# Kernel optimization log

Measured on AMD Instinct MI355X. Metric: run time of the kernel, lower is better.

## Reference

```python
import jax, jax.numpy as jnp
import numpy as np

N_HEADS = 12

def setup_inputs() -> dict:
    key = jax.random.key(0)
    ks = jax.random.split(key, 3)
    B, C, T = 4, 768, 2048
    x = jax.random.normal(ks[0], (B, C, T), dtype=jnp.float32)
    mask = jnp.ones((B, 1, 1, T), dtype=jnp.int32)  # all valid; masked_fill where mask==0
    Wqkv = jax.random.normal(ks[1], (3 * C, C), dtype=jnp.float32) * 0.02
    bqkv = jnp.zeros((3 * C,), dtype=jnp.float32)
    Wout = jax.random.normal(ks[2], (C, C), dtype=jnp.float32) * 0.02
    bout = jnp.zeros((C,), dtype=jnp.float32)
    return {"x": x, "mask": mask, "Wqkv": Wqkv, "bqkv": bqkv, "Wout": Wout, "bout": bout}


def reference(x, mask, Wqkv, bqkv, Wout, bout):
    B, C, T = x.shape
    H = N_HEADS
    d = C // H
    scale = 1.0 / jnp.sqrt(jnp.asarray(d, x.dtype))
    # 1x1 Conv1d == per-timestep matmul over channels
    qkv = jnp.einsum('oc,bct->bot', Wqkv, x) + bqkv[None, :, None]  # [B,3C,T]
    # channel dim splits as [3, H, d] per the torch view(B,3,H,d,T)
    qkv = qkv.reshape(B, 3, H, d, T).transpose(0, 1, 2, 4, 3)       # [B,3,H,T,d]
    q, k, v = qkv[:, 0], qkv[:, 1], qkv[:, 2]
    score = jnp.einsum('bhtd,bhsd->bhts', q, k) * scale             # [B,H,T,T]
    score = jnp.where(mask == 0, jnp.asarray(-10000.0, score.dtype), score)
    attn = jax.nn.softmax(score, axis=-1)  # dropout: eval mode (identity)
    o = jnp.einsum('bhts,bhsd->bhtd', attn, v)                      # [B,H,T,d]
    o = o.transpose(0, 1, 3, 2).reshape(B, C, T)                    # [B,C,T]
    return jnp.einsum('oc,bct->bot', Wout, o) + bout[None, :, None]
```

## Files before the change

### kernel.cpp

```cpp
#include <hip/hip_runtime.h>
#include <hip/hip_bf16.h>
#include <stdint.h>

#define B_   4
#define C_   768
#define T_   2048
#define H_   12
#define D_   64
#define O3_  2304

typedef __attribute__((ext_vector_type(4))) float f32x4;
typedef __attribute__((ext_vector_type(8))) short bf16x8;

__device__ __forceinline__ unsigned short f2bf(float f) {
  union { float f; unsigned int u; } v; v.f = f;
  unsigned int r = v.u + 0x7fffu + ((v.u >> 16) & 1u);
  return (unsigned short)(r >> 16);
}

__device__ __forceinline__ unsigned int pack2bf(float a, float b) {
  __hip_bfloat162 h2 = __float22bfloat162_rn(make_float2(a, b));
  union { __hip_bfloat162 h; unsigned int u; } cv; cv.h = h2;
  return cv.u;
}

__device__ __forceinline__ float fexp2(float x) {
#if __has_builtin(__builtin_amdgcn_exp2f)
  return __builtin_amdgcn_exp2f(x);
#else
  return exp2f(x);
#endif
}

__device__ __forceinline__ void async16(const void* g, void* lds) {
#if __has_builtin(__builtin_amdgcn_global_load_lds)
  __builtin_amdgcn_global_load_lds((const __attribute__((address_space(1))) void*)g,
                                   (__attribute__((address_space(3))) void*)lds, 16, 0, 0);
#else
  int lane = threadIdx.x & 63;
  *((uint4*)((char*)lds + lane * 16)) = *((const uint4*)g);
#endif
}


__global__ void cvt_f32_bf16(const float* __restrict__ in,
                             unsigned short* __restrict__ out, int n4) {
  int i = blockIdx.x * 256 + threadIdx.x;
  if (i < n4) {
    float4 f = ((const float4*)in)[i];
    ushort4 o;
    o.x = f2bf(f.x); o.y = f2bf(f.y); o.z = f2bf(f.z); o.w = f2bf(f.w);
    ((ushort4*)out)[i] = o;
  }
}

__global__ void make_bias(const int* __restrict__ mask, float* __restrict__ mbias, int n) {
  int i = blockIdx.x * 256 + threadIdx.x;
  if (i < n) mbias[i] = (mask[i] == 0) ? -14426.950408f : 0.0f;
}

__global__ void transpose_x(const float* __restrict__ x,
                            unsigned short* __restrict__ xT) {
  __shared__ unsigned short tile[32][33];
  int b = blockIdx.z;
  int c0 = blockIdx.y * 32;
  int t0 = blockIdx.x * 32;
  int tid = threadIdx.x;
  {
    int cl = tid >> 3;
    int tl = (tid & 7) * 4;
    float4 f = *(const float4*)(x + ((size_t)b * C_ + c0 + cl) * T_ + t0 + tl);
    tile[tl + 0][cl] = f2bf(f.x);
    tile[tl + 1][cl] = f2bf(f.y);
    tile[tl + 2][cl] = f2bf(f.z);
    tile[tl + 3][cl] = f2bf(f.w);
  }
  __syncthreads();
  {
    int tl = tid >> 3;
    int cl = (tid & 7) * 4;
    ushort4 o;
    o.x = tile[tl][cl + 0]; o.y = tile[tl][cl + 1];
    o.z = tile[tl][cl + 2]; o.w = tile[tl][cl + 3];
    *(ushort4*)(xT + ((size_t)b * T_ + t0 + tl) * C_ + c0 + cl) = o;
  }
}

__global__ __launch_bounds__(256)
void gemm_qkv(const unsigned short* __restrict__ xT,
              const unsigned short* __restrict__ W1,
              const float* __restrict__ bqkv,
              unsigned short* __restrict__ Qb,
              unsigned short* __restrict__ Kb,
              unsigned short* __restrict__ Vb) {
  __shared__ unsigned short sA[2][128 * 32];
  __shared__ unsigned short sB[2][128 * 32];

  const int b   = blockIdx.z;
  const int o0  = blockIdx.y * 128;
  const int t0  = blockIdx.x * 128;
  const int tid = threadIdx.x;
  const int wave = tid >> 6, lane = tid & 63;
  const int q = lane >> 4, ln = lane & 15;
  const int tw = wave >> 1, ow = wave & 1;

  const unsigned short* Ax = xT + (size_t)b * T_ * C_;
  const int srow = lane >> 2;
  const int scol = (lane & 3) * 8;

  const f32x4 ZERO = {0.f, 0.f, 0.f, 0.f};
  f32x4 acc[4][4];
#pragma unroll
  for (int mi = 0; mi < 4; ++mi)
#pragma unroll
    for (int ni = 0; ni < 4; ++ni) acc[mi][ni] = ZERO;

#pragma unroll
  for (int j = 0; j < 2; ++j) {
    const int chunk = wave * 2 + j;
    const int row = chunk * 16 + srow;
    async16(Ax + (size_t)(t0 + row) * C_ + scol, &sA[0][chunk * 512]);
    async16(W1 + (size_t)(o0 + row) * C_ + scol, &sB[0][chunk * 512]);
  }

  for (int i = 0; i < 24; ++i) {
    const int buf = i & 1;
    __syncthreads();
    if (i < 23) {
      const int k0 = (i + 1) * 32;
#pragma unroll
      for (int j = 0; j < 2; ++j) {
        const int chunk = wave * 2 + j;
        const int row = chunk * 16 + srow;
        async16(Ax + (size_t)(t0 + row) * C_ + k0 + scol, &sA[buf ^ 1][chunk * 512]);
        async16(W1 + (size_t)(o0 + row) * C_ + k0 + scol, &sB[buf ^ 1][chunk * 512]);
      }
    }

    bf16x8 aF[4], bF[4];
#pragma unroll
    for (int mi = 0; mi < 4; ++mi)
      aF[mi] = *(const bf16x8*)(&sA[buf][(tw * 64 + mi * 16 + ln) * 32 + q * 8]);
#pragma unroll
    for (int ni = 0; ni < 4; ++ni)
      bF[ni] = *(const bf16x8*)(&sB[buf][(ow * 64 + ni * 16 + ln) * 32 + q * 8]);
#pragma unroll
    for (int mi = 0; mi < 4; ++mi)
#pragma unroll
      for (int ni = 0; ni < 4; ++ni)
        acc[mi][ni] = __builtin_amdgcn_mfma_f32_16x16x32_bf16(aF[mi], bF[ni], acc[mi][ni], 0, 0, 0);
  }

  const float QSCL = 0.125f * 1.44269504f;
#pragma unroll
  for (int ni = 0; ni < 4; ++ni) {
    const int o = o0 + ow * 64 + ni * 16 + ln;
    const float bias = bqkv[o];
    const int which = o / C_;
    const int rem = o - which * C_;
    const int bh = b * H_ + (rem >> 6);
    const int dd = rem & 63;
#pragma unroll
    for (int mi = 0; mi < 4; ++mi) {
      const int tb = t0 + tw * 64 + mi * 16 + q * 4;
      f32x4 v = acc[mi][ni];
      if (which == 0) {
#pragma unroll
        for (int r = 0; r < 4; ++r)
          Qb[((size_t)bh * T_ + tb + r) * D_ + dd] = f2bf((v[r] + bias) * QSCL);
      } else if (which == 1) {
#pragma unroll
        for (int r = 0; r < 4; ++r) {
          const int s = tb + r;
          const int cp = (dd >> 3) ^ (s & 7);
          Kb[((size_t)bh * T_ + s) * 64 + (cp << 3) + (dd & 7)] = f2bf(v[r] + bias);
        }
      } else {
        const int tile = tb >> 6, si = tb & 63;
        const int cp = (si >> 3) ^ (dd & 7);
        ushort4 pk;
        pk.x = f2bf(v[0] + bias);
        pk.y = f2bf(v[1] + bias);
        pk.z = f2bf(v[2] + bias);
        pk.w = f2bf(v[3] + bias);
        *(ushort4*)(Vb + (((size_t)bh * 32 + tile) * 64 + dd) * 64 + (cp << 3) + (si & 7)) = pk;
      }
    }
  }
}

__global__ __launch_bounds__(256, 3)
void attn(const unsigned short* __restrict__ Qb,
          const unsigned short* __restrict__ Kb,
          const unsigned short* __restrict__ Vb,
          const float* __restrict__ mbias,
          unsigned short* __restrict__ Ob) {
  __shared__ __align__(16) char smem[53248];
  unsigned short* sK0 = (unsigned short*)smem;
  unsigned short* sV0 = (unsigned short*)(smem + 16384);

  const int id = blockIdx.x;
  const int bh = id % 48;
  const int tblk = id / 48;
  const int b = bh / H_, h = bh % H_;
  const int tid = threadIdx.x, wave = tid >> 6, lane = tid & 63;
  const int q = lane >> 4, ln = lane & 15;
  const int wj = wave & 1, si = wave >> 1;
  const int t0w = tblk * 128 + wj * 64;
  unsigned short* sPw = (unsigned short*)(smem + 32768 + wave * 5120);

  bf16x8 Qa[4][2];
#pragma unroll
  for (int tt = 0; tt < 4; ++tt) {
    const unsigned short* qrow = Qb + ((size_t)bh * T_ + t0w + tt * 16 + ln) * D_;
    Qa[tt][0] = *(const bf16x8*)(qrow + q * 8);
    Qa[tt][1] = *(const bf16x8*)(qrow + 32 + q * 8);
  }

  const f32x4 ZERO = {0.f, 0.f, 0.f, 0.f};
  f32x4 Oacc[4][4];
  f32x4 lacc[4];
#pragma unroll
  for (int dt = 0; dt < 4; ++dt)
#pragma unroll
    for (int tt = 0; tt < 4; ++tt) Oacc[dt][tt] = ZERO;
#pragma unroll
  for (int tt = 0; tt < 4; ++tt) lacc[tt] = ZERO;

  const short one_s = (ln == 0) ? (short)0x3F80 : (short)0;
  bf16x8 ones;
#pragma unroll
  for (int j = 0; j < 8; ++j) ones[j] = one_s;

  const unsigned short* gK = Kb + (size_t)bh * T_ * 64;
  const unsigned short* gV = Vb + (size_t)bh * 32 * 4096;

#pragma unroll
  for (int j = 0; j < 2; ++j) {
    const int chunk = wave * 2 + j;
    async16(gK + chunk * 512 + lane * 8, sK0 + chunk * 512);
    async16(gV + chunk * 512 + lane * 8, sV0 + chunk * 512);
  }

  for (int it = 0; it < 32; ++it) {
    const int buf = it & 1;
    __syncthreads();
    if (it < 31) {
      const unsigned short* k = gK + (it + 1) * 4096;
      const unsigned short* v = gV + (it + 1) * 4096;
      unsigned short* dK = sK0 + (buf ^ 1) * 4096;
      unsigned short* dV = sV0 + (buf ^ 1) * 4096;
#pragma unroll
      for (int j = 0; j < 2; ++j) {
        const int chunk = wave * 2 + j;
        async16(k + chunk * 512 + lane * 8, dK + chunk * 512);
        async16(v + chunk * 512 + lane * 8, dV + chunk * 512);
      }
    }

    const int s0 = it * 64;
    const float bvl = mbias[b * T_ + s0 + lane];
    const bool anymask = (__ballot(bvl != 0.0f) != 0ull);
    const unsigned short* sKc = sK0 + buf * 4096;
    const unsigned short* sVc = sV0 + buf * 4096;

#pragma unroll
    for (int sb = 0; sb < 2; ++sb) {
      const unsigned short* krow = sKc + (si * 32 + sb * 16 + ln) * 64;
      bf16x8 kf0 = *(const bf16x8*)(krow + ((q ^ (ln & 7)) << 3));
      bf16x8 kf1 = *(const bf16x8*)(krow + (((4 + q) ^ (ln & 7)) << 3));
      f32x4 bb = ZERO;
      if (anymask) bb = *(const f32x4*)(mbias + b * T_ + s0 + si * 32 + sb * 16 + q * 4);
#pragma unroll
      for (int tt = 0; tt < 4; ++tt) {
        f32x4 p0 = __builtin_amdgcn_mfma_f32_16x16x32_bf16(kf0, Qa[tt][0], ZERO, 0, 0, 0);
        f32x4 sc = __builtin_amdgcn_mfma_f32_16x16x32_bf16(kf1, Qa[tt][1], p0, 0, 0, 0);
        if (anymask) {
#pragma unroll
          for (int r = 0; r < 4; ++r) sc[r] += bb[r];
        }
        uint2 w;
        w.x = pack2bf(fexp2(sc[0]), fexp2(sc[1]));
        w.y = pack2bf(fexp2(sc[2]), fexp2(sc[3]));
        *(uint2*)(sPw + (tt * 16 + ln) * 40 + sb * 16 + q * 4) = w;
      }
    }

    bf16x8 vf[4];
#pragma unroll
    for (int dt = 0; dt < 4; ++dt)
      vf[dt] = *(const bf16x8*)(sVc + (dt * 16 + ln) * 64 +
                                (((si * 4 + q) ^ (ln & 7)) << 3));
#pragma unroll
    for (int tt = 0; tt < 4; ++tt) {
      bf16x8 pf = *(const bf16x8*)(sPw + (tt * 16 + ln) * 40 + q * 8);
      lacc[tt] = __builtin_amdgcn_mfma_f32_16x16x32_bf16(ones, pf, lacc[tt], 0, 0, 0);
#pragma unroll
      for (int dt = 0; dt < 4; ++dt)
        Oacc[dt][tt] = __builtin_amdgcn_mfma_f32_16x16x32_bf16(vf[dt], pf, Oacc[dt][tt], 0, 0, 0);
    }
  }

  __syncthreads();
  float* fbuf = (float*)smem;
  float* lbuf = (float*)(smem + 34816);
  if (si == 1) {
#pragma unroll
    for (int tt = 0; tt < 4; ++tt) {
#pragma unroll
      for (int dt = 0; dt < 4; ++dt)
        *(f32x4*)(fbuf + ((size_t)(wj * 64 + tt * 16 + ln)) * 68 + dt * 16 + q * 4) = Oacc[dt][tt];
      if (q == 0) lbuf[wj * 64 + tt * 16 + ln] = lacc[tt][0];
    }
  }
  __syncthreads();
  if (si == 0) {
#pragma unroll
    for (int tt = 0; tt < 4; ++tt) {
      const float lv = __shfl(lacc[tt][0], ln, 64) + lbuf[wj * 64 + tt * 16 + ln];
      const float inv = 1.0f / lv;
      const int t = t0w + tt * 16 + ln;
#pragma unroll
      for (int dt = 0; dt < 4; ++dt) {
        f32x4 o = Oacc[dt][tt];
        f32x4 p = *(const f32x4*)(fbuf + ((size_t)(wj * 64 + tt * 16 + ln)) * 68 + dt * 16 + q * 4);
        ushort4 pk;
        pk.x = f2bf((o[0] + p[0]) * inv);
        pk.y = f2bf((o[1] + p[1]) * inv);
        pk.z = f2bf((o[2] + p[2]) * inv);
        pk.w = f2bf((o[3] + p[3]) * inv);
        *(ushort4*)(Ob + ((size_t)b * T_ + t) * C_ + h * D_ + dt * 16 + q * 4) = pk;
      }
    }
  }
}

__global__ __launch_bounds__(256)
void gemm_out(const unsigned short* __restrict__ Ob,
              const unsigned short* __restrict__ W2,
              const float* __restrict__ bout,
              float* __restrict__ out) {
  __shared__ unsigned short sA[2][128 * 32];
  __shared__ unsigned short sB[2][128 * 32];

  const int b   = blockIdx.z;
  const int o0  = blockIdx.y * 128;
  const int t0  = blockIdx.x * 128;
  const int tid = threadIdx.x;
  const int wave = tid >> 6, lane = tid & 63;
  const int q = lane >> 4, ln = lane & 15;
  const int tw = wave >> 1, ow = wave & 1;

  const unsigned short* Bo = Ob + (size_t)b * T_ * C_;
  const int srow = lane >> 2;
  const int scol = (lane & 3) * 8;

  const f32x4 ZERO = {0.f, 0.f, 0.f, 0.f};
  f32x4 acc[4][4];
#pragma unroll
  for (int mi = 0; mi < 4; ++mi)
#pragma unroll
    for (int ni = 0; ni < 4; ++ni) acc[mi][ni] = ZERO;

#pragma unroll
  for (int j = 0; j < 2; ++j) {
    const int chunk = wave * 2 + j;
    const int row = chunk * 16 + srow;
    async16(W2 + (size_t)(o0 + row) * C_ + scol, &sA[0][chunk * 512]);
    async16(Bo + (size_t)(t0 + row) * C_ + scol, &sB[0][chunk * 512]);
  }

  for (int i = 0; i < 24; ++i) {
    const int buf = i & 1;
    __syncthreads();
    if (i < 23) {
      const int k0 = (i + 1) * 32;
#pragma unroll
      for (int j = 0; j < 2; ++j) {
        const int chunk = wave * 2 + j;
        const int row = chunk * 16 + srow;
        async16(W2 + (size_t)(o0 + row) * C_ + k0 + scol, &sA[buf ^ 1][chunk * 512]);
        async16(Bo + (size_t)(t0 + row) * C_ + k0 + scol, &sB[buf ^ 1][chunk * 512]);
      }
    }

    bf16x8 aF[4], bF[4];
#pragma unroll
    for (int mi = 0; mi < 4; ++mi)
      aF[mi] = *(const bf16x8*)(&sA[buf][(tw * 64 + mi * 16 + ln) * 32 + q * 8]);
#pragma unroll
    for (int ni = 0; ni < 4; ++ni)
      bF[ni] = *(const bf16x8*)(&sB[buf][(ow * 64 + ni * 16 + ln) * 32 + q * 8]);
#pragma unroll
    for (int mi = 0; mi < 4; ++mi)
#pragma unroll
      for (int ni = 0; ni < 4; ++ni)
        acc[mi][ni] = __builtin_amdgcn_mfma_f32_16x16x32_bf16(aF[mi], bF[ni], acc[mi][ni], 0, 0, 0);
  }

#pragma unroll
  for (int mi = 0; mi < 4; ++mi) {
    const int ob = o0 + tw * 64 + mi * 16 + q * 4;
#pragma unroll
    for (int ni = 0; ni < 4; ++ni) {
      const int t = t0 + ow * 64 + ni * 16 + ln;
      f32x4 v = acc[mi][ni];
#pragma unroll
      for (int r = 0; r < 4; ++r)
        out[((size_t)b * C_ + ob + r) * T_ + t] = v[r] + bout[ob + r];
    }
  }
}


extern "C" void kernel_launch(void* const* d_in, const int* in_sizes, int n_in,
                              void* d_out, int out_size, void* d_ws, size_t ws_size,
                              hipStream_t stream) {
  (void)in_sizes; (void)n_in; (void)out_size; (void)ws_size;
  const float* x    = (const float*)d_in[0];
  const int*   mask = (const int*)d_in[1];
  const float* Wqkv = (const float*)d_in[2];
  const float* bqkv = (const float*)d_in[3];
  const float* Wout = (const float*)d_in[4];
  const float* bout = (const float*)d_in[5];
  float* out = (float*)d_out;

  const size_t szHead = (size_t)B_ * H_ * T_ * D_;
  const size_t szBTC  = (size_t)B_ * T_ * C_;
  unsigned short* Qb  = (unsigned short*)d_ws;
  unsigned short* Kb  = Qb + szHead;
  unsigned short* Vb  = Kb + szHead;
  unsigned short* Ob  = Vb + szHead;
  unsigned short* xT  = Ob + szBTC;
  unsigned short* W1b = xT + szBTC;
  unsigned short* W2b = W1b + (size_t)O3_ * C_;
  float* mbias        = (float*)(W2b + (size_t)C_ * C_);

  cvt_f32_bf16<<<dim3((O3_ * C_ / 4 + 255) / 256), 256, 0, stream>>>(Wqkv, W1b, O3_ * C_ / 4);
  cvt_f32_bf16<<<dim3((C_ * C_ / 4 + 255) / 256), 256, 0, stream>>>(Wout, W2b, C_ * C_ / 4);
  make_bias<<<dim3((B_ * T_ + 255) / 256), 256, 0, stream>>>(mask, mbias, B_ * T_);
  transpose_x<<<dim3(T_ / 32, C_ / 32, B_), 256, 0, stream>>>(x, xT);
  gemm_qkv<<<dim3(T_ / 128, O3_ / 128, B_), 256, 0, stream>>>(xT, W1b, bqkv, Qb, Kb, Vb);
  attn<<<dim3(768), 256, 0, stream>>>(Qb, Kb, Vb, mbias, Ob);
  gemm_out<<<dim3(T_ / 128, C_ / 128, B_), 256, 0, stream>>>(Ob, W2b, bout, out);
}
```

Baseline: 236.3 us.

## Keep softmax probabilities in registers via permlane swaps instead of LDS round-trip

```diff
diff --git a/kernel.cpp b/kernel.cpp
--- a/kernel.cpp
+++ b/kernel.cpp
@@ -195,7 +195,7 @@
           const unsigned short* __restrict__ Vb,
           const float* __restrict__ mbias,
           unsigned short* __restrict__ Ob) {
-  __shared__ __align__(16) char smem[53248];
+  __shared__ __align__(16) char smem[32768];
   unsigned short* sK0 = (unsigned short*)smem;
   unsigned short* sV0 = (unsigned short*)(smem + 16384);
 
@@ -205,27 +205,25 @@
   const int b = bh / H_, h = bh % H_;
   const int tid = threadIdx.x, wave = tid >> 6, lane = tid & 63;
   const int q = lane >> 4, ln = lane & 15;
-  const int wj = wave & 1, si = wave >> 1;
-  const int t0w = tblk * 128 + wj * 64;
-  unsigned short* sPw = (unsigned short*)(smem + 32768 + wave * 5120);
-
-  bf16x8 Qa[4][2];
-#pragma unroll
-  for (int tt = 0; tt < 4; ++tt) {
+  const int t0w = tblk * 128 + wave * 32;
+
+  bf16x8 Qa[2][2];
+#pragma unroll
+  for (int tt = 0; tt < 2; ++tt) {
     const unsigned short* qrow = Qb + ((size_t)bh * T_ + t0w + tt * 16 + ln) * D_;
     Qa[tt][0] = *(const bf16x8*)(qrow + q * 8);
     Qa[tt][1] = *(const bf16x8*)(qrow + 32 + q * 8);
   }
 
   const f32x4 ZERO = {0.f, 0.f, 0.f, 0.f};
-  f32x4 Oacc[4][4];
-  f32x4 lacc[4];
+  f32x4 Oacc[4][2];
+  f32x4 lacc[2];
 #pragma unroll
   for (int dt = 0; dt < 4; ++dt)
 #pragma unroll
-    for (int tt = 0; tt < 4; ++tt) Oacc[dt][tt] = ZERO;
-#pragma unroll
-  for (int tt = 0; tt < 4; ++tt) lacc[tt] = ZERO;
+    for (int tt = 0; tt < 2; ++tt) Oacc[dt][tt] = ZERO;
+#pragma unroll
+  for (int tt = 0; tt < 2; ++tt) lacc[tt] = ZERO;
 
   const short one_s = (ln == 0) ? (short)0x3F80 : (short)0;
   bf16x8 ones;
@@ -264,73 +262,78 @@
     const unsigned short* sKc = sK0 + buf * 4096;
     const unsigned short* sVc = sV0 + buf * 4096;
 
-#pragma unroll
-    for (int sb = 0; sb < 2; ++sb) {
-      const unsigned short* krow = sKc + (si * 32 + sb * 16 + ln) * 64;
-      bf16x8 kf0 = *(const bf16x8*)(krow + ((q ^ (ln & 7)) << 3));
-      bf16x8 kf1 = *(const bf16x8*)(krow + (((4 + q) ^ (ln & 7)) << 3));
-      f32x4 bb = ZERO;
-      if (anymask) bb = *(const f32x4*)(mbias + b * T_ + s0 + si * 32 + sb * 16 + q * 4);
-#pragma unroll
-      for (int tt = 0; tt < 4; ++tt) {
-        f32x4 p0 = __builtin_amdgcn_mfma_f32_16x16x32_bf16(kf0, Qa[tt][0], ZERO, 0, 0, 0);
-        f32x4 sc = __builtin_amdgcn_mfma_f32_16x16x32_bf16(kf1, Qa[tt][1], p0, 0, 0, 0);
-        if (anymask) {
-#pragma unroll
-          for (int r = 0; r < 4; ++r) sc[r] += bb[r];
+    bf16x8 pf[2][2];
+#pragma unroll
+    for (int kc = 0; kc < 2; ++kc) {
+      bf16x8 kf[2][2];
+#pragma unroll
+      for (int sb = 0; sb < 2; ++sb) {
+        const unsigned short* krow = sKc + (kc * 32 + sb * 16 + ln) * 64;
+        kf[sb][0] = *(const bf16x8*)(krow + ((q ^ (ln & 7)) << 3));
+        kf[sb][1] = *(const bf16x8*)(krow + (((4 + q) ^ (ln & 7)) << 3));
+      }
+#pragma unroll
+      for (int tt = 0; tt < 2; ++tt) {
+        f32x4 sc[2];
+#pragma unroll
+        for (int sb = 0; sb < 2; ++sb) {
+          f32x4 p0 = __builtin_amdgcn_mfma_f32_16x16x32_bf16(kf[sb][0], Qa[tt][0], ZERO, 0, 0, 0);
+          sc[sb]   = __builtin_amdgcn_mfma_f32_16x16x32_bf16(kf[sb][1], Qa[tt][1], p0, 0, 0, 0);
+          if (anymask) {
+            f32x4 bb = *(const f32x4*)(mbias + b * T_ + s0 + kc * 32 + sb * 16 + q * 4);
+#pragma unroll
+            for (int r = 0; r < 4; ++r) sc[sb][r] += bb[r];
+          }
         }
-        uint2 w;
-        w.x = pack2bf(fexp2(sc[0]), fexp2(sc[1]));
-        w.y = pack2bf(fexp2(sc[2]), fexp2(sc[3]));
-        *(uint2*)(sPw + (tt * 16 + ln) * 40 + sb * 16 + q * 4) = w;
-      }
-    }
-
-    bf16x8 vf[4];
-#pragma unroll
-    for (int dt = 0; dt < 4; ++dt)
-      vf[dt] = *(const bf16x8*)(sVc + (dt * 16 + ln) * 64 +
-                                (((si * 4 + q) ^ (ln & 7)) << 3));
-#pragma unroll
-    for (int tt = 0; tt < 4; ++tt) {
-      bf16x8 pf = *(const bf16x8*)(sPw + (tt * 16 + ln) * 40 + q * 8);
-      lacc[tt] = __builtin_amdgcn_mfma_f32_16x16x32_bf16(ones, pf, lacc[tt], 0, 0, 0);
-#pragma unroll
-      for (int dt = 0; dt < 4; ++dt)
-        Oacc[dt][tt] = __builtin_amdgcn_mfma_f32_16x16x32_bf16(vf[dt], pf, Oacc[dt][tt], 0, 0, 0);
-    }
-  }
-
-  __syncthreads();
-  float* fbuf = (float*)smem;
-  float* lbuf = (float*)(smem + 34816);
-  if (si == 1) {
-#pragma unroll
-    for (int tt = 0; tt < 4; ++tt) {
-#pragma unroll
-      for (int dt = 0; dt < 4; ++dt)
-        *(f32x4*)(fbuf + ((size_t)(wj * 64 + tt * 16 + ln)) * 68 + dt * 16 + q * 4) = Oacc[dt][tt];
-      if (q == 0) lbuf[wj * 64 + tt * 16 + ln] = lacc[tt][0];
-    }
-  }
-  __syncthreads();
-  if (si == 0) {
-#pragma unroll
-    for (int tt = 0; tt < 4; ++tt) {
-      const float lv = __shfl(lacc[tt][0], ln, 64) + lbuf[wj * 64 + tt * 16 + ln];
-      const float inv = 1.0f / lv;
-      const int t = t0w + tt * 16 + ln;
-#pragma unroll
-      for (int dt = 0; dt < 4; ++dt) {
-        f32x4 o = Oacc[dt][tt];
-        f32x4 p = *(const f32x4*)(fbuf + ((size_t)(wj * 64 + tt * 16 + ln)) * 68 + dt * 16 + q * 4);
-        ushort4 pk;
-        pk.x = f2bf((o[0] + p[0]) * inv);
-        pk.y = f2bf((o[1] + p[1]) * inv);
-        pk.z = f2bf((o[2] + p[2]) * inv);
-        pk.w = f2bf((o[3] + p[3]) * inv);
-        *(ushort4*)(Ob + ((size_t)b * T_ + t) * C_ + h * D_ + dt * 16 + q * 4) = pk;
-      }
+        unsigned int A0 = pack2bf(fexp2(sc[0][0]), fexp2(sc[0][1]));
+        unsigned int B0 = pack2bf(fexp2(sc[0][2]), fexp2(sc[0][3]));
+        unsigned int C0 = pack2bf(fexp2(sc[1][0]), fexp2(sc[1][1]));
+        unsigned int E0 = pack2bf(fexp2(sc[1][2]), fexp2(sc[1][3]));
+        asm volatile("v_permlane32_swap_b32 %0, %1" : "+v"(A0), "+v"(C0));
+        asm volatile("v_permlane16_swap_b32 %0, %1" : "+v"(A0), "+v"(C0));
+        asm volatile("v_permlane32_swap_b32 %0, %1" : "+v"(B0), "+v"(E0));
+        asm volatile("v_permlane16_swap_b32 %0, %1" : "+v"(B0), "+v"(E0));
+        union { bf16x8 v; unsigned int u[4]; } P;
+        P.u[0] = A0;
+        P.u[1] = B0;
+        P.u[2] = C0;
+        P.u[3] = E0;
+        pf[tt][kc] = P.v;
+      }
+    }
+
+#pragma unroll
+    for (int dt = 0; dt < 4; ++dt) {
+#pragma unroll
+      for (int kc = 0; kc < 2; ++kc) {
+        bf16x8 vf = *(const bf16x8*)(sVc + (dt * 16 + ln) * 64 +
+                                     (((kc * 4 + q) ^ (ln & 7)) << 3));
+#pragma unroll
+        for (int tt = 0; tt < 2; ++tt)
+          Oacc[dt][tt] = __builtin_amdgcn_mfma_f32_16x16x32_bf16(vf, pf[tt][kc], Oacc[dt][tt], 0, 0, 0);
+      }
+    }
+#pragma unroll
+    for (int kc = 0; kc < 2; ++kc)
+#pragma unroll
+      for (int tt = 0; tt < 2; ++tt)
+        lacc[tt] = __builtin_amdgcn_mfma_f32_16x16x32_bf16(ones, pf[tt][kc], lacc[tt], 0, 0, 0);
+  }
+
+#pragma unroll
+  for (int tt = 0; tt < 2; ++tt) {
+    const float lv = __shfl(lacc[tt][0], ln, 64);
+    const float inv = 1.0f / lv;
+    const int t = t0w + tt * 16 + ln;
+#pragma unroll
+    for (int dt = 0; dt < 4; ++dt) {
+      f32x4 o = Oacc[dt][tt];
+      ushort4 pk;
+      pk.x = f2bf(o[0] * inv);
+      pk.y = f2bf(o[1] * inv);
+      pk.z = f2bf(o[2] * inv);
+      pk.w = f2bf(o[3] * inv);
+      *(ushort4*)(Ob + ((size_t)b * T_ + t) * C_ + h * D_ + dt * 16 + q * 4) = pk;
     }
   }
 }
```

Result: faster. 228.4 us (-3.4%).
